# Kernel optimization log

Measured on AMD Instinct MI355X. Metric: run time of the kernel, lower is better.

## Reference

```python
import jax, jax.numpy as jnp
import numpy as np

D_MODEL = 1024
D_FF = 2048
NA = 4
NB = 4
E = NA * NB
B = 2
S = 1024


def setup_inputs() -> dict:
    key = jax.random.key(0)
    ks = jax.random.split(key, 8)
    s = 0.02
    x = jax.random.normal(ks[0], (B, S, D_MODEL), dtype=jnp.float32)
    # stacked per-expert FFN params (torch Linear stored as [in, out] here)
    W1 = (jax.random.normal(ks[1], (E, D_MODEL, 2 * D_FF), dtype=jnp.float32) * s)
    b1 = jnp.zeros((E, 2 * D_FF), dtype=jnp.float32)
    W2 = (jax.random.normal(ks[2], (E, D_FF, D_MODEL), dtype=jnp.float32) * s)
    b2 = jnp.zeros((E, D_MODEL), dtype=jnp.float32)
    Wga = jax.random.normal(ks[3], (D_MODEL, NA), dtype=jnp.float32) * s
    bga = jnp.zeros((NA,), dtype=jnp.float32)
    Wgb = jax.random.normal(ks[4], (D_MODEL, NB), dtype=jnp.float32) * s
    bgb = jnp.zeros((NB,), dtype=jnp.float32)
    return {"x": x, "W1": W1, "b1": b1, "W2": W2, "b2": b2,
            "Wga": Wga, "bga": bga, "Wgb": Wgb, "bgb": bgb}


def reference(x, W1, b1, W2, b2, Wga, bga, Wgb, bgb):
    b, s, d = x.shape
    xf = x.reshape(b * s, d)                     # [T, d]
    probs_A = jax.nn.softmax(xf @ Wga + bga, axis=-1)   # [T, NA]
    probs_B = jax.nn.softmax(xf @ Wgb + bgb, axis=-1)   # [T, NB]
    idx_A = jnp.argmax(probs_A, axis=-1)
    idx_B = jnp.argmax(probs_B, axis=-1)
    oh_A = jax.nn.one_hot(idx_A, NA, dtype=xf.dtype)
    oh_B = jax.nn.one_hot(idx_B, NB, dtype=xf.dtype)
    aux_A = NA * jnp.sum(probs_A.mean(0) * oh_A.mean(0))
    aux_B = NB * jnp.sum(probs_B.mean(0) * oh_B.mean(0))
    total_aux = aux_A + aux_B

    # flattened Cartesian expert index per token
    e_idx = idx_A * NB + idx_B                   # [T]

    # run all experts densely, then select per token (vectorized dispatch)
    h = jnp.einsum('td,edf->etf', xf, W1) + b1[:, None, :]   # [E, T, 2*d_ff]
    a, g = jnp.split(h, 2, axis=-1)
    act = a * jax.nn.silu(g)                                  # [E, T, d_ff]
    y = jnp.einsum('etf,efd->etd', act, W2) + b2[:, None, :]  # [E, T, d]
    oh_E = jax.nn.one_hot(e_idx, E, dtype=xf.dtype)           # [T, E]
    out = jnp.einsum('te,etd->td', oh_E, y)                   # [T, d]
    return out.reshape(b, s, d), total_aux
```

## Files before the change

### kernel.cpp

```cpp
#include <hip/hip_runtime.h>
#include <cstdint>
#include <cstddef>

#define TOKENS 2048
#define DM 1024
#define DFF 2048
#define HC 4096
#define NE 16
#define BM 128

typedef __bf16 bf16x8 __attribute__((ext_vector_type(8)));
typedef float floatx4 __attribute__((ext_vector_type(4)));

static __device__ __forceinline__ unsigned short f2bf(float f) {
    union { float f; unsigned int u; } v; v.f = f;
    unsigned int r = v.u + 0x7fffu + ((v.u >> 16) & 1u);
    return (unsigned short)(r >> 16);
}

union BF8 { bf16x8 v; unsigned short u[8]; };

__global__ __launch_bounds__(256) void moe_gating(
    const float* __restrict__ x, const float* __restrict__ Wga, const float* __restrict__ bga,
    const float* __restrict__ Wgb, const float* __restrict__ bgb,
    float* __restrict__ probsA, float* __restrict__ probsB, int* __restrict__ e_idx)
{
    int wv = threadIdx.x >> 6, lane = threadIdx.x & 63;
    int t = blockIdx.x * 4 + wv;
    const float* xr = x + (size_t)t * DM;
    double aA[4] = {0.,0.,0.,0.}, aB[4] = {0.,0.,0.,0.};
    for (int k = lane; k < DM; k += 64) {
        double xv = (double)xr[k];
        float4 wa = *(const float4*)(Wga + k * 4);
        float4 wb = *(const float4*)(Wgb + k * 4);
        aA[0] += xv * wa.x; aA[1] += xv * wa.y; aA[2] += xv * wa.z; aA[3] += xv * wa.w;
        aB[0] += xv * wb.x; aB[1] += xv * wb.y; aB[2] += xv * wb.z; aB[3] += xv * wb.w;
    }
    #pragma unroll
    for (int off = 32; off >= 1; off >>= 1) {
        #pragma unroll
        for (int j = 0; j < 4; ++j) {
            aA[j] += __shfl_xor(aA[j], off);
            aB[j] += __shfl_xor(aB[j], off);
        }
    }
    if (lane == 0) {
        double lA[4], lB[4];
        #pragma unroll
        for (int j = 0; j < 4; ++j) {
            lA[j] = aA[j] + (double)bga[j];
            lB[j] = aB[j] + (double)bgb[j];
        }
        int ia = 0, ib = 0;
        #pragma unroll
        for (int j = 1; j < 4; ++j) {
            if (lA[j] > lA[ia]) ia = j;
            if (lB[j] > lB[ib]) ib = j;
        }
        double sA = 0., sB = 0., pA[4], pB[4];
        #pragma unroll
        for (int j = 0; j < 4; ++j) {
            pA[j] = exp(lA[j] - lA[ia]); sA += pA[j];
            pB[j] = exp(lB[j] - lB[ib]); sB += pB[j];
        }
        float4 oa, ob;
        oa.x = (float)(pA[0]/sA); oa.y = (float)(pA[1]/sA);
        oa.z = (float)(pA[2]/sA); oa.w = (float)(pA[3]/sA);
        ob.x = (float)(pB[0]/sB); ob.y = (float)(pB[1]/sB);
        ob.z = (float)(pB[2]/sB); ob.w = (float)(pB[3]/sB);
        *(float4*)(probsA + t * 4) = oa;
        *(float4*)(probsB + t * 4) = ob;
        e_idx[t] = ia * 4 + ib;
    }
}

__global__ __launch_bounds__(256) void moe_stats(
    const float* __restrict__ probsA, const float* __restrict__ probsB,
    const int* __restrict__ e_idx,
    int* __restrict__ countE, int* __restrict__ offsets, float* __restrict__ aux_out)
{
    __shared__ float sA[4], sB[4];
    __shared__ int cA[4], cB[4], cE[16];
    int tid = threadIdx.x;
    if (tid < 4) { sA[tid] = 0.f; sB[tid] = 0.f; cA[tid] = 0; cB[tid] = 0; }
    if (tid < 16) cE[tid] = 0;
    __syncthreads();
    float lA[4] = {0,0,0,0}, lB[4] = {0,0,0,0};
    for (int t = tid; t < TOKENS; t += 256) {
        float4 pa = *(const float4*)(probsA + t * 4);
        float4 pb = *(const float4*)(probsB + t * 4);
        lA[0] += pa.x; lA[1] += pa.y; lA[2] += pa.z; lA[3] += pa.w;
        lB[0] += pb.x; lB[1] += pb.y; lB[2] += pb.z; lB[3] += pb.w;
        int e = e_idx[t];
        atomicAdd(&cE[e], 1);
        atomicAdd(&cA[e >> 2], 1);
        atomicAdd(&cB[e & 3], 1);
    }
    #pragma unroll
    for (int j = 0; j < 4; ++j) {
        atomicAdd(&sA[j], lA[j]);
        atomicAdd(&sB[j], lB[j]);
    }
    __syncthreads();
    if (tid == 0) {
        int acc = 0;
        for (int e = 0; e < NE; ++e) { offsets[e] = acc; countE[e] = cE[e]; acc += cE[e]; }
        offsets[NE] = acc;
        float invT = 1.0f / (float)TOKENS;
        float auxA = 0.f, auxB = 0.f;
        for (int j = 0; j < 4; ++j) {
            auxA += (sA[j] * invT) * ((float)cA[j] * invT);
            auxB += (sB[j] * invT) * ((float)cB[j] * invT);
        }
        aux_out[0] = 4.0f * auxA + 4.0f * auxB;
    }
}

__global__ __launch_bounds__(256) void moe_slot(const int* __restrict__ e_idx,
                                                const int* __restrict__ offsets,
                                                int* __restrict__ cursor, int* __restrict__ perm)
{
    int t = blockIdx.x * 256 + threadIdx.x;
    int e = e_idx[t];
    int s = offsets[e] + atomicAdd(&cursor[e], 1);
    perm[s] = t;
}

__global__ __launch_bounds__(256) void moe_gather(const float* __restrict__ x,
                                                  const int* __restrict__ perm,
                                                  unsigned short* __restrict__ Xg)
{
    int s = blockIdx.x;
    int t = perm[s];
    int i = threadIdx.x * 4;
    float4 v = *(const float4*)(x + (size_t)t * DM + i);
    ushort4 o;
    o.x = f2bf(v.x); o.y = f2bf(v.y); o.z = f2bf(v.z); o.w = f2bf(v.w);
    *(ushort4*)(Xg + (size_t)s * DM + i) = o;
}

__global__ __launch_bounds__(256) void moe_ffn1(
    const unsigned short* __restrict__ Xg, const float* __restrict__ W1,
    const float* __restrict__ b1, const int* __restrict__ countE,
    const int* __restrict__ offsets, unsigned short* __restrict__ actbuf)
{
    int e = blockIdx.y;
    int cnt = countE[e];
    if (cnt == 0) return;
    int base = offsets[e];
    int n0 = blockIdx.x * 64;
    __shared__ __align__(16) unsigned short Xs[2 * BM * 40];
    int tid = threadIdx.x, wv = tid >> 6, lane = tid & 63;
    int quad = lane >> 4, l15 = lane & 15;
    const float* W1e = W1 + (size_t)e * DM * HC;
    int col = n0 + wv * 16 + l15;
    const float* pa = W1e + col;
    const float* pg = W1e + DFF + col;
    float ba = b1[e * HC + col];
    float bg = b1[e * HC + DFF + col];
    int row = tid >> 2, kc = tid & 3;

    for (int m0 = blockIdx.z * BM; m0 < cnt; m0 += 2 * BM) {
        floatx4 acc[8][2];
        #pragma unroll
        for (int i = 0; i < 8; ++i) {
            acc[i][0] = floatx4{0.f,0.f,0.f,0.f};
            acc[i][1] = floatx4{0.f,0.f,0.f,0.f};
        }
        #pragma unroll
        for (int p = 0; p < 2; ++p) {
            int r = row + p * 64;
            uint4 v = {0u,0u,0u,0u};
            int m = m0 + r;
            if (m < cnt) v = *(const uint4*)(Xg + (size_t)(base + m) * DM + kc * 8);
            *(uint4*)(Xs + r * 40 + kc * 8) = v;
        }
        float curA[8], curG[8], nxtA[8], nxtG[8];
        {
            const float* qa = pa + (size_t)(quad * 8) * HC;
            const float* qg = pg + (size_t)(quad * 8) * HC;
            #pragma unroll
            for (int j = 0; j < 8; ++j) { curA[j] = qa[(size_t)j * HC]; curG[j] = qg[(size_t)j * HC]; }
        }
        __syncthreads();
        for (int ks = 0; ks < DM / 32; ++ks) {
            int buf = ks & 1;
            if (ks + 1 < DM / 32) {
                int k0n = (ks + 1) * 32;
                #pragma unroll
                for (int p = 0; p < 2; ++p) {
                    int r = row + p * 64;
                    uint4 v = {0u,0u,0u,0u};
                    int m = m0 + r;
                    if (m < cnt) v = *(const uint4*)(Xg + (size_t)(base + m) * DM + k0n + kc * 8);
                    *(uint4*)(Xs + (buf ^ 1) * (BM * 40) + r * 40 + kc * 8) = v;
                }
            }
            bf16x8 af[8];
            #pragma unroll
            for (int i = 0; i < 8; ++i)
                af[i] = *(const bf16x8*)(Xs + buf * (BM * 40) + (i * 16 + l15) * 40 + quad * 8);
            if (ks + 1 < DM / 32) {
                const float* qa = pa + (size_t)((ks + 1) * 32 + quad * 8) * HC;
                const float* qg = pg + (size_t)((ks + 1) * 32 + quad * 8) * HC;
                #pragma unroll
                for (int j = 0; j < 8; ++j) { nxtA[j] = qa[(size_t)j * HC]; nxtG[j] = qg[(size_t)j * HC]; }
            }
            BF8 fa, fg;
            #pragma unroll
            for (int j = 0; j < 8; ++j) { fa.u[j] = f2bf(curA[j]); fg.u[j] = f2bf(curG[j]); }
            #pragma unroll
            for (int i = 0; i < 8; ++i) {
                acc[i][0] = __builtin_amdgcn_mfma_f32_16x16x32_bf16(af[i], fa.v, acc[i][0], 0, 0, 0);
                acc[i][1] = __builtin_amdgcn_mfma_f32_16x16x32_bf16(af[i], fg.v, acc[i][1], 0, 0, 0);
            }
            #pragma unroll
            for (int j = 0; j < 8; ++j) { curA[j] = nxtA[j]; curG[j] = nxtG[j]; }
            __syncthreads();
        }
        #pragma unroll
        for (int i = 0; i < 8; ++i) {
            #pragma unroll
            for (int r = 0; r < 4; ++r) {
                int mr = m0 + i * 16 + quad * 4 + r;
                if (mr < cnt) {
                    float a = acc[i][0][r] + ba;
                    float g = acc[i][1][r] + bg;
                    float sg = 1.0f / (1.0f + __expf(-g));
                    actbuf[(size_t)(base + mr) * DFF + col] = f2bf(a * (g * sg));
                }
            }
        }
    }
}

__global__ __launch_bounds__(256) void moe_ffn2(
    const unsigned short* __restrict__ actbuf, const float* __restrict__ W2,
    const float* __restrict__ b2, const int* __restrict__ countE,
    const int* __restrict__ offsets, const int* __restrict__ perm,
    float* __restrict__ out)
{
    int e = blockIdx.y;
    int cnt = countE[e];
    if (cnt == 0) return;
    int base = offsets[e];
    int n0 = blockIdx.x * 64;
    __shared__ __align__(16) unsigned short As[2 * BM * 40];
    int tid = threadIdx.x, wv = tid >> 6, lane = tid & 63;
    int quad = lane >> 4, l15 = lane & 15;
    const float* W2e = W2 + (size_t)e * DFF * DM;
    int col = n0 + wv * 16 + l15;
    const float* pb = W2e + col;
    float bias = b2[e * DM + col];
    int row = tid >> 2, kc = tid & 3;

    for (int m0 = blockIdx.z * BM; m0 < cnt; m0 += 2 * BM) {
        floatx4 acc[8];
        #pragma unroll
        for (int i = 0; i < 8; ++i) acc[i] = floatx4{0.f,0.f,0.f,0.f};
        #pragma unroll
        for (int p = 0; p < 2; ++p) {
            int r = row + p * 64;
            uint4 v = {0u,0u,0u,0u};
            int m = m0 + r;
            if (m < cnt) v = *(const uint4*)(actbuf + (size_t)(base + m) * DFF + kc * 8);
            *(uint4*)(As + r * 40 + kc * 8) = v;
        }
        float curB[8], nxtB[8];
        {
            const float* qb = pb + (size_t)(quad * 8) * DM;
            #pragma unroll
            for (int j = 0; j < 8; ++j) curB[j] = qb[(size_t)j * DM];
        }
        __syncthreads();
        for (int ks = 0; ks < DFF / 32; ++ks) {
            int buf = ks & 1;
            if (ks + 1 < DFF / 32) {
                int k0n = (ks + 1) * 32;
                #pragma unroll
                for (int p = 0; p < 2; ++p) {
                    int r = row + p * 64;
                    uint4 v = {0u,0u,0u,0u};
                    int m = m0 + r;
                    if (m < cnt) v = *(const uint4*)(actbuf + (size_t)(base + m) * DFF + k0n + kc * 8);
                    *(uint4*)(As + (buf ^ 1) * (BM * 40) + r * 40 + kc * 8) = v;
                }
            }
            bf16x8 af[8];
            #pragma unroll
            for (int i = 0; i < 8; ++i)
                af[i] = *(const bf16x8*)(As + buf * (BM * 40) + (i * 16 + l15) * 40 + quad * 8);
            if (ks + 1 < DFF / 32) {
                const float* qb = pb + (size_t)((ks + 1) * 32 + quad * 8) * DM;
                #pragma unroll
                for (int j = 0; j < 8; ++j) nxtB[j] = qb[(size_t)j * DM];
            }
            BF8 fb;
            #pragma unroll
            for (int j = 0; j < 8; ++j) fb.u[j] = f2bf(curB[j]);
            #pragma unroll
            for (int i = 0; i < 8; ++i)
                acc[i] = __builtin_amdgcn_mfma_f32_16x16x32_bf16(af[i], fb.v, acc[i], 0, 0, 0);
            #pragma unroll
            for (int j = 0; j < 8; ++j) curB[j] = nxtB[j];
            __syncthreads();
        }
        #pragma unroll
        for (int i = 0; i < 8; ++i) {
            #pragma unroll
            for (int r = 0; r < 4; ++r) {
                int mr = m0 + i * 16 + quad * 4 + r;
                if (mr < cnt) {
                    int t = perm[base + mr];
                    out[(size_t)t * DM + col] = acc[i][r] + bias;
                }
            }
        }
    }
}

extern "C" void kernel_launch(void* const* d_in, const int* in_sizes, int n_in,
                              void* d_out, int out_size, void* d_ws, size_t ws_size,
                              hipStream_t stream)
{
    (void)in_sizes; (void)n_in; (void)out_size; (void)ws_size;
    const float* x   = (const float*)d_in[0];
    const float* W1  = (const float*)d_in[1];
    const float* b1  = (const float*)d_in[2];
    const float* W2  = (const float*)d_in[3];
    const float* b2  = (const float*)d_in[4];
    const float* Wga = (const float*)d_in[5];
    const float* bga = (const float*)d_in[6];
    const float* Wgb = (const float*)d_in[7];
    const float* bgb = (const float*)d_in[8];
    float* out = (float*)d_out;

    char* ws = (char*)d_ws;
    int*   countE  = (int*)(ws + 0);
    int*   cursor  = (int*)(ws + 64);
    int*   offsets = (int*)(ws + 256);
    int*   e_idx   = (int*)(ws + 512);
    int*   perm    = (int*)(ws + 8704);
    float* probsA  = (float*)(ws + 16896);
    float* probsB  = (float*)(ws + 49664);
    unsigned short* Xg     = (unsigned short*)(ws + 131072);
    unsigned short* actbuf = (unsigned short*)(ws + (size_t)8 * 1024 * 1024);

    hipMemsetAsync(ws, 0, 256, stream);
    moe_gating<<<TOKENS / 4, 256, 0, stream>>>(x, Wga, bga, Wgb, bgb,
                                               probsA, probsB, e_idx);
    moe_stats<<<1, 256, 0, stream>>>(probsA, probsB, e_idx, countE, offsets,
                                     out + (size_t)TOKENS * DM);
    moe_slot<<<TOKENS / 256, 256, 0, stream>>>(e_idx, offsets, cursor, perm);
    moe_gather<<<TOKENS, 256, 0, stream>>>(x, perm, Xg);
    moe_ffn1<<<dim3(DFF / 64, NE, 2), 256, 0, stream>>>(Xg, W1, b1, countE, offsets, actbuf);
    moe_ffn2<<<dim3(DM / 64, NE, 2), 256, 0, stream>>>(actbuf, W2, b2, countE, offsets, perm, out);
}
```

Baseline: 578.9 us.

## Merge M-split blocks into 512-thread blocks sharing weight loads, defer LDS stores

The grid z-split over token tiles is replaced by a single 512-thread block with a 256-row tile. Two wave groups split the M dimension, so each weight column is fetched once per block instead of once per z-block. The next tile's global loads are now issued before the MFMAs and written to LDS only after them, behind a lighter barrier. bf16 conversion uses native casts instead of the manual rounding helper. The cost is fewer blocks in flight, which lowers parallelism when an expert has few tokens, and more register pressure per block.

```diff
diff --git a/kernel.cpp b/kernel.cpp
--- a/kernel.cpp
+++ b/kernel.cpp
@@ -7,7 +7,7 @@
 #define DFF 2048
 #define HC 4096
 #define NE 16
-#define BM 128
+#define BM 256
 
 typedef __bf16 bf16x8 __attribute__((ext_vector_type(8)));
 typedef float floatx4 __attribute__((ext_vector_type(4)));
@@ -18,7 +18,11 @@
     return (unsigned short)(r >> 16);
 }
 
-union BF8 { bf16x8 v; unsigned short u[8]; };
+static __device__ __forceinline__ void lds_barrier() {
+    asm volatile("s_waitcnt lgkmcnt(0)" ::: "memory");
+    __builtin_amdgcn_s_barrier();
+    __builtin_amdgcn_sched_barrier(0);
+}
 
 __global__ __launch_bounds__(256) void moe_gating(
     const float* __restrict__ x, const float* __restrict__ Wga, const float* __restrict__ bga,
@@ -139,7 +143,7 @@
     *(ushort4*)(Xg + (size_t)s * DM + i) = o;
 }
 
-__global__ __launch_bounds__(256) void moe_ffn1(
+__global__ __launch_bounds__(512) void moe_ffn1(
     const unsigned short* __restrict__ Xg, const float* __restrict__ W1,
     const float* __restrict__ b1, const int* __restrict__ countE,
     const int* __restrict__ offsets, unsigned short* __restrict__ actbuf)
@@ -152,28 +156,29 @@
     __shared__ __align__(16) unsigned short Xs[2 * BM * 40];
     int tid = threadIdx.x, wv = tid >> 6, lane = tid & 63;
     int quad = lane >> 4, l15 = lane & 15;
+    int wvM = wv >> 2, wvN = wv & 3;
     const float* W1e = W1 + (size_t)e * DM * HC;
-    int col = n0 + wv * 16 + l15;
+    int col = n0 + wvN * 16 + l15;
     const float* pa = W1e + col;
     const float* pg = W1e + DFF + col;
     float ba = b1[e * HC + col];
     float bg = b1[e * HC + DFF + col];
     int row = tid >> 2, kc = tid & 3;
 
-    for (int m0 = blockIdx.z * BM; m0 < cnt; m0 += 2 * BM) {
+    for (int m0 = 0; m0 < cnt; m0 += BM) {
         floatx4 acc[8][2];
         #pragma unroll
         for (int i = 0; i < 8; ++i) {
             acc[i][0] = floatx4{0.f,0.f,0.f,0.f};
             acc[i][1] = floatx4{0.f,0.f,0.f,0.f};
         }
-        #pragma unroll
-        for (int p = 0; p < 2; ++p) {
-            int r = row + p * 64;
-            uint4 v = {0u,0u,0u,0u};
-            int m = m0 + r;
-            if (m < cnt) v = *(const uint4*)(Xg + (size_t)(base + m) * DM + kc * 8);
-            *(uint4*)(Xs + r * 40 + kc * 8) = v;
+        {
+            uint4 av0 = {0u,0u,0u,0u}, av1 = {0u,0u,0u,0u};
+            int ma = m0 + row, mb = m0 + row + 128;
+            if (ma < cnt) av0 = *(const uint4*)(Xg + (size_t)(base + ma) * DM + kc * 8);
+            if (mb < cnt) av1 = *(const uint4*)(Xg + (size_t)(base + mb) * DM + kc * 8);
+            *(uint4*)(Xs + row * 40 + kc * 8) = av0;
+            *(uint4*)(Xs + (row + 128) * 40 + kc * 8) = av1;
         }
         float curA[8], curG[8], nxtA[8], nxtG[8];
         {
@@ -182,47 +187,46 @@
             #pragma unroll
             for (int j = 0; j < 8; ++j) { curA[j] = qa[(size_t)j * HC]; curG[j] = qg[(size_t)j * HC]; }
         }
-        __syncthreads();
+        lds_barrier();
         for (int ks = 0; ks < DM / 32; ++ks) {
             int buf = ks & 1;
-            if (ks + 1 < DM / 32) {
+            uint4 nv0 = {0u,0u,0u,0u}, nv1 = {0u,0u,0u,0u};
+            bool more = (ks + 1 < DM / 32);
+            if (more) {
                 int k0n = (ks + 1) * 32;
-                #pragma unroll
-                for (int p = 0; p < 2; ++p) {
-                    int r = row + p * 64;
-                    uint4 v = {0u,0u,0u,0u};
-                    int m = m0 + r;
-                    if (m < cnt) v = *(const uint4*)(Xg + (size_t)(base + m) * DM + k0n + kc * 8);
-                    *(uint4*)(Xs + (buf ^ 1) * (BM * 40) + r * 40 + kc * 8) = v;
-                }
-            }
-            bf16x8 af[8];
-            #pragma unroll
-            for (int i = 0; i < 8; ++i)
-                af[i] = *(const bf16x8*)(Xs + buf * (BM * 40) + (i * 16 + l15) * 40 + quad * 8);
-            if (ks + 1 < DM / 32) {
+                int ma = m0 + row, mb = m0 + row + 128;
+                if (ma < cnt) nv0 = *(const uint4*)(Xg + (size_t)(base + ma) * DM + k0n + kc * 8);
+                if (mb < cnt) nv1 = *(const uint4*)(Xg + (size_t)(base + mb) * DM + k0n + kc * 8);
                 const float* qa = pa + (size_t)((ks + 1) * 32 + quad * 8) * HC;
                 const float* qg = pg + (size_t)((ks + 1) * 32 + quad * 8) * HC;
                 #pragma unroll
                 for (int j = 0; j < 8; ++j) { nxtA[j] = qa[(size_t)j * HC]; nxtG[j] = qg[(size_t)j * HC]; }
             }
-            BF8 fa, fg;
-            #pragma unroll
-            for (int j = 0; j < 8; ++j) { fa.u[j] = f2bf(curA[j]); fg.u[j] = f2bf(curG[j]); }
+            bf16x8 af[8];
+            #pragma unroll
+            for (int i = 0; i < 8; ++i)
+                af[i] = *(const bf16x8*)(Xs + buf * (BM * 40) + (wvM * 128 + i * 16 + l15) * 40 + quad * 8);
+            bf16x8 fa, fg;
+            #pragma unroll
+            for (int j = 0; j < 8; ++j) { fa[j] = (__bf16)curA[j]; fg[j] = (__bf16)curG[j]; }
             #pragma unroll
             for (int i = 0; i < 8; ++i) {
-                acc[i][0] = __builtin_amdgcn_mfma_f32_16x16x32_bf16(af[i], fa.v, acc[i][0], 0, 0, 0);
-                acc[i][1] = __builtin_amdgcn_mfma_f32_16x16x32_bf16(af[i], fg.v, acc[i][1], 0, 0, 0);
-            }
-            #pragma unroll
-            for (int j = 0; j < 8; ++j) { curA[j] = nxtA[j]; curG[j] = nxtG[j]; }
-            __syncthreads();
+                acc[i][0] = __builtin_amdgcn_mfma_f32_16x16x32_bf16(af[i], fa, acc[i][0], 0, 0, 0);
+                acc[i][1] = __builtin_amdgcn_mfma_f32_16x16x32_bf16(af[i], fg, acc[i][1], 0, 0, 0);
+            }
+            if (more) {
+                *(uint4*)(Xs + (buf ^ 1) * (BM * 40) + row * 40 + kc * 8) = nv0;
+                *(uint4*)(Xs + (buf ^ 1) * (BM * 40) + (row + 128) * 40 + kc * 8) = nv1;
+                #pragma unroll
+                for (int j = 0; j < 8; ++j) { curA[j] = nxtA[j]; curG[j] = nxtG[j]; }
+            }
+            lds_barrier();
         }
         #pragma unroll
         for (int i = 0; i < 8; ++i) {
             #pragma unroll
             for (int r = 0; r < 4; ++r) {
-                int mr = m0 + i * 16 + quad * 4 + r;
+                int mr = m0 + wvM * 128 + i * 16 + quad * 4 + r;
                 if (mr < cnt) {
                     float a = acc[i][0][r] + ba;
                     float g = acc[i][1][r] + bg;
@@ -234,7 +238,7 @@
     }
 }
 
-__global__ __launch_bounds__(256) void moe_ffn2(
+__global__ __launch_bounds__(512) void moe_ffn2(
     const unsigned short* __restrict__ actbuf, const float* __restrict__ W2,
     const float* __restrict__ b2, const int* __restrict__ countE,
     const int* __restrict__ offsets, const int* __restrict__ perm,
@@ -248,23 +252,24 @@
     __shared__ __align__(16) unsigned short As[2 * BM * 40];
     int tid = threadIdx.x, wv = tid >> 6, lane = tid & 63;
     int quad = lane >> 4, l15 = lane & 15;
+    int wvM = wv >> 2, wvN = wv & 3;
     const float* W2e = W2 + (size_t)e * DFF * DM;
-    int col = n0 + wv * 16 + l15;
+    int col = n0 + wvN * 16 + l15;
     const float* pb = W2e + col;
     float bias = b2[e * DM + col];
     int row = tid >> 2, kc = tid & 3;
 
-    for (int m0 = blockIdx.z * BM; m0 < cnt; m0 += 2 * BM) {
+    for (int m0 = 0; m0 < cnt; m0 += BM) {
         floatx4 acc[8];
         #pragma unroll
         for (int i = 0; i < 8; ++i) acc[i] = floatx4{0.f,0.f,0.f,0.f};
-        #pragma unroll
-        for (int p = 0; p < 2; ++p) {
-            int r = row + p * 64;
-            uint4 v = {0u,0u,0u,0u};
-            int m = m0 + r;
-            if (m < cnt) v = *(const uint4*)(actbuf + (size_t)(base + m) * DFF + kc * 8);
-            *(uint4*)(As + r * 40 + kc * 8) = v;
+        {
+            uint4 av0 = {0u,0u,0u,0u}, av1 = {0u,0u,0u,0u};
+            int ma = m0 + row, mb = m0 + row + 128;
+            if (ma < cnt) av0 = *(const uint4*)(actbuf + (size_t)(base + ma) * DFF + kc * 8);
+            if (mb < cnt) av1 = *(const uint4*)(actbuf + (size_t)(base + mb) * DFF + kc * 8);
+            *(uint4*)(As + row * 40 + kc * 8) = av0;
+            *(uint4*)(As + (row + 128) * 40 + kc * 8) = av1;
         }
         float curB[8], nxtB[8];
         {
@@ -272,44 +277,43 @@
             #pragma unroll
             for (int j = 0; j < 8; ++j) curB[j] = qb[(size_t)j * DM];
         }
-        __syncthreads();
+        lds_barrier();
         for (int ks = 0; ks < DFF / 32; ++ks) {
             int buf = ks & 1;
-            if (ks + 1 < DFF / 32) {
+            uint4 nv0 = {0u,0u,0u,0u}, nv1 = {0u,0u,0u,0u};
+            bool more = (ks + 1 < DFF / 32);
+            if (more) {
                 int k0n = (ks + 1) * 32;
-                #pragma unroll
-                for (int p = 0; p < 2; ++p) {
-                    int r = row + p * 64;
-                    uint4 v = {0u,0u,0u,0u};
-                    int m = m0 + r;
-                    if (m < cnt) v = *(const uint4*)(actbuf + (size_t)(base + m) * DFF + k0n + kc * 8);
-                    *(uint4*)(As + (buf ^ 1) * (BM * 40) + r * 40 + kc * 8) = v;
-                }
-            }
-            bf16x8 af[8];
-            #pragma unroll
-            for (int i = 0; i < 8; ++i)
-                af[i] = *(const bf16x8*)(As + buf * (BM * 40) + (i * 16 + l15) * 40 + quad * 8);
-            if (ks + 1 < DFF / 32) {
+                int ma = m0 + row, mb = m0 + row + 128;
+                if (ma < cnt) nv0 = *(const uint4*)(actbuf + (size_t)(base + ma) * DFF + k0n + kc * 8);
+                if (mb < cnt) nv1 = *(const uint4*)(actbuf + (size_t)(base + mb) * DFF + k0n + kc * 8);
                 const float* qb = pb + (size_t)((ks + 1) * 32 + quad * 8) * DM;
                 #pragma unroll
                 for (int j = 0; j < 8; ++j) nxtB[j] = qb[(size_t)j * DM];
             }
-            BF8 fb;
-            #pragma unroll
-            for (int j = 0; j < 8; ++j) fb.u[j] = f2bf(curB[j]);
+            bf16x8 af[8];
             #pragma unroll
             for (int i = 0; i < 8; ++i)
-                acc[i] = __builtin_amdgcn_mfma_f32_16x16x32_bf16(af[i], fb.v, acc[i], 0, 0, 0);
-            #pragma unroll
-            for (int j = 0; j < 8; ++j) curB[j] = nxtB[j];
-            __syncthreads();
+                af[i] = *(const bf16x8*)(As + buf * (BM * 40) + (wvM * 128 + i * 16 + l15) * 40 + quad * 8);
+            bf16x8 fb;
+            #pragma unroll
+            for (int j = 0; j < 8; ++j) fb[j] = (__bf16)curB[j];
+            #pragma unroll
+            for (int i = 0; i < 8; ++i)
+                acc[i] = __builtin_amdgcn_mfma_f32_16x16x32_bf16(af[i], fb, acc[i], 0, 0, 0);
+            if (more) {
+                *(uint4*)(As + (buf ^ 1) * (BM * 40) + row * 40 + kc * 8) = nv0;
+                *(uint4*)(As + (buf ^ 1) * (BM * 40) + (row + 128) * 40 + kc * 8) = nv1;
+                #pragma unroll
+                for (int j = 0; j < 8; ++j) curB[j] = nxtB[j];
+            }
+            lds_barrier();
         }
         #pragma unroll
         for (int i = 0; i < 8; ++i) {
             #pragma unroll
             for (int r = 0; r < 4; ++r) {
-                int mr = m0 + i * 16 + quad * 4 + r;
+                int mr = m0 + wvM * 128 + i * 16 + quad * 4 + r;
                 if (mr < cnt) {
                     int t = perm[base + mr];
                     out[(size_t)t * DM + col] = acc[i][r] + bias;
@@ -353,6 +357,6 @@
                                      out + (size_t)TOKENS * DM);
     moe_slot<<<TOKENS / 256, 256, 0, stream>>>(e_idx, offsets, cursor, perm);
     moe_gather<<<TOKENS, 256, 0, stream>>>(x, perm, Xg);
-    moe_ffn1<<<dim3(DFF / 64, NE, 2), 256, 0, stream>>>(Xg, W1, b1, countE, offsets, actbuf);
-    moe_ffn2<<<dim3(DM / 64, NE, 2), 256, 0, stream>>>(actbuf, W2, b2, countE, offsets, perm, out);
-}
+    moe_ffn1<<<dim3(DFF / 64, NE), 512, 0, stream>>>(Xg, W1, b1, countE, offsets, actbuf);
+    moe_ffn2<<<dim3(DM / 64, NE), 512, 0, stream>>>(actbuf, W2, b2, countE, offsets, perm, out);
+}
```

Result: faster. 535.7 us (-7.5%).

## Enlarge FFN GEMM tiles to 256x128 with 512 threads and deeper weight prefetch

Applied to the files above, without the earlier changes.

Both expert FFN kernels now run 512-thread blocks covering 256 token rows and 128 output columns, and the M-split grid dimension is dropped. The block index is remapped so that neighbouring blocks share an expert, which should help L2 reuse of the weights. Weights are prefetched two k-steps ahead, and LDS stores are deferred until after the MFMAs behind a lightweight waitcnt+barrier. The aim is less redundant weight streaming and better latency hiding, at the cost of fewer blocks (256 and 128) and higher register pressure from the doubled accumulators.

```diff
diff --git a/kernel.cpp b/kernel.cpp
--- a/kernel.cpp
+++ b/kernel.cpp
@@ -7,7 +7,7 @@
 #define DFF 2048
 #define HC 4096
 #define NE 16
-#define BM 128
+#define BM 256
 
 typedef __bf16 bf16x8 __attribute__((ext_vector_type(8)));
 typedef float floatx4 __attribute__((ext_vector_type(4)));
@@ -18,7 +18,11 @@
     return (unsigned short)(r >> 16);
 }
 
-union BF8 { bf16x8 v; unsigned short u[8]; };
+static __device__ __forceinline__ void lds_barrier() {
+    asm volatile("s_waitcnt lgkmcnt(0)" ::: "memory");
+    __builtin_amdgcn_s_barrier();
+    __builtin_amdgcn_sched_barrier(0);
+}
 
 __global__ __launch_bounds__(256) void moe_gating(
     const float* __restrict__ x, const float* __restrict__ Wga, const float* __restrict__ bga,
@@ -139,16 +143,19 @@
     *(ushort4*)(Xg + (size_t)s * DM + i) = o;
 }
 
-__global__ __launch_bounds__(256) void moe_ffn1(
+#define NS1 (DM / 32)
+__global__ __launch_bounds__(512, 2) void moe_ffn1(
     const unsigned short* __restrict__ Xg, const float* __restrict__ W1,
     const float* __restrict__ b1, const int* __restrict__ countE,
     const int* __restrict__ offsets, unsigned short* __restrict__ actbuf)
 {
-    int e = blockIdx.y;
+    int id = blockIdx.y * 16 + blockIdx.x;
+    int lid = (id & 7) * 32 + (id >> 3);
+    int e = lid >> 4;
+    int n0 = (lid & 15) * 128;
     int cnt = countE[e];
     if (cnt == 0) return;
     int base = offsets[e];
-    int n0 = blockIdx.x * 64;
     __shared__ __align__(16) unsigned short Xs[2 * BM * 40];
     int tid = threadIdx.x, wv = tid >> 6, lane = tid & 63;
     int quad = lane >> 4, l15 = lane & 15;
@@ -160,66 +167,75 @@
     float bg = b1[e * HC + DFF + col];
     int row = tid >> 2, kc = tid & 3;
 
-    for (int m0 = blockIdx.z * BM; m0 < cnt; m0 += 2 * BM) {
-        floatx4 acc[8][2];
-        #pragma unroll
-        for (int i = 0; i < 8; ++i) {
+    for (int m0 = 0; m0 < cnt; m0 += BM) {
+        floatx4 acc[16][2];
+        #pragma unroll
+        for (int i = 0; i < 16; ++i) {
             acc[i][0] = floatx4{0.f,0.f,0.f,0.f};
             acc[i][1] = floatx4{0.f,0.f,0.f,0.f};
         }
         #pragma unroll
         for (int p = 0; p < 2; ++p) {
-            int r = row + p * 64;
-            uint4 v = {0u,0u,0u,0u};
-            int m = m0 + r;
+            int m = m0 + row + p * 128;
+            uint4 v; v.x = 0u; v.y = 0u; v.z = 0u; v.w = 0u;
             if (m < cnt) v = *(const uint4*)(Xg + (size_t)(base + m) * DM + kc * 8);
-            *(uint4*)(Xs + r * 40 + kc * 8) = v;
-        }
-        float curA[8], curG[8], nxtA[8], nxtG[8];
+            *(uint4*)(Xs + (row + p * 128) * 40 + kc * 8) = v;
+        }
+        float curA[8], curG[8], nxtA[8], nxtG[8], n2A[8], n2G[8];
         {
             const float* qa = pa + (size_t)(quad * 8) * HC;
             const float* qg = pg + (size_t)(quad * 8) * HC;
             #pragma unroll
             for (int j = 0; j < 8; ++j) { curA[j] = qa[(size_t)j * HC]; curG[j] = qg[(size_t)j * HC]; }
-        }
-        __syncthreads();
-        for (int ks = 0; ks < DM / 32; ++ks) {
+            const float* ra = pa + (size_t)(32 + quad * 8) * HC;
+            const float* rg = pg + (size_t)(32 + quad * 8) * HC;
+            #pragma unroll
+            for (int j = 0; j < 8; ++j) { nxtA[j] = ra[(size_t)j * HC]; nxtG[j] = rg[(size_t)j * HC]; }
+        }
+        lds_barrier();
+        for (int ks = 0; ks < NS1; ++ks) {
             int buf = ks & 1;
-            if (ks + 1 < DM / 32) {
+            bool w1 = (ks + 1 < NS1), w2 = (ks + 2 < NS1);
+            uint4 RA[2];
+            if (w1) {
                 int k0n = (ks + 1) * 32;
                 #pragma unroll
                 for (int p = 0; p < 2; ++p) {
-                    int r = row + p * 64;
-                    uint4 v = {0u,0u,0u,0u};
-                    int m = m0 + r;
-                    if (m < cnt) v = *(const uint4*)(Xg + (size_t)(base + m) * DM + k0n + kc * 8);
-                    *(uint4*)(Xs + (buf ^ 1) * (BM * 40) + r * 40 + kc * 8) = v;
+                    int m = m0 + row + p * 128;
+                    RA[p].x = 0u; RA[p].y = 0u; RA[p].z = 0u; RA[p].w = 0u;
+                    if (m < cnt) RA[p] = *(const uint4*)(Xg + (size_t)(base + m) * DM + k0n + kc * 8);
                 }
             }
-            bf16x8 af[8];
-            #pragma unroll
-            for (int i = 0; i < 8; ++i)
-                af[i] = *(const bf16x8*)(Xs + buf * (BM * 40) + (i * 16 + l15) * 40 + quad * 8);
-            if (ks + 1 < DM / 32) {
-                const float* qa = pa + (size_t)((ks + 1) * 32 + quad * 8) * HC;
-                const float* qg = pg + (size_t)((ks + 1) * 32 + quad * 8) * HC;
-                #pragma unroll
-                for (int j = 0; j < 8; ++j) { nxtA[j] = qa[(size_t)j * HC]; nxtG[j] = qg[(size_t)j * HC]; }
-            }
-            BF8 fa, fg;
-            #pragma unroll
-            for (int j = 0; j < 8; ++j) { fa.u[j] = f2bf(curA[j]); fg.u[j] = f2bf(curG[j]); }
-            #pragma unroll
-            for (int i = 0; i < 8; ++i) {
-                acc[i][0] = __builtin_amdgcn_mfma_f32_16x16x32_bf16(af[i], fa.v, acc[i][0], 0, 0, 0);
-                acc[i][1] = __builtin_amdgcn_mfma_f32_16x16x32_bf16(af[i], fg.v, acc[i][1], 0, 0, 0);
-            }
-            #pragma unroll
-            for (int j = 0; j < 8; ++j) { curA[j] = nxtA[j]; curG[j] = nxtG[j]; }
-            __syncthreads();
-        }
-        #pragma unroll
-        for (int i = 0; i < 8; ++i) {
+            if (w2) {
+                const float* qa = pa + (size_t)((ks + 2) * 32 + quad * 8) * HC;
+                const float* qg = pg + (size_t)((ks + 2) * 32 + quad * 8) * HC;
+                #pragma unroll
+                for (int j = 0; j < 8; ++j) { n2A[j] = qa[(size_t)j * HC]; n2G[j] = qg[(size_t)j * HC]; }
+            }
+            bf16x8 fa, fg;
+            #pragma unroll
+            for (int j = 0; j < 8; ++j) { fa[j] = (__bf16)curA[j]; fg[j] = (__bf16)curG[j]; }
+            #pragma unroll
+            for (int i = 0; i < 16; ++i) {
+                bf16x8 af = *(const bf16x8*)(Xs + buf * (BM * 40) + (i * 16 + l15) * 40 + quad * 8);
+                acc[i][0] = __builtin_amdgcn_mfma_f32_16x16x32_bf16(af, fa, acc[i][0], 0, 0, 0);
+                acc[i][1] = __builtin_amdgcn_mfma_f32_16x16x32_bf16(af, fg, acc[i][1], 0, 0, 0);
+            }
+            if (w1) {
+                #pragma unroll
+                for (int p = 0; p < 2; ++p)
+                    *(uint4*)(Xs + (buf ^ 1) * (BM * 40) + (row + p * 128) * 40 + kc * 8) = RA[p];
+                #pragma unroll
+                for (int j = 0; j < 8; ++j) { curA[j] = nxtA[j]; curG[j] = nxtG[j]; }
+            }
+            if (w2) {
+                #pragma unroll
+                for (int j = 0; j < 8; ++j) { nxtA[j] = n2A[j]; nxtG[j] = n2G[j]; }
+            }
+            lds_barrier();
+        }
+        #pragma unroll
+        for (int i = 0; i < 16; ++i) {
             #pragma unroll
             for (int r = 0; r < 4; ++r) {
                 int mr = m0 + i * 16 + quad * 4 + r;
@@ -234,17 +250,20 @@
     }
 }
 
-__global__ __launch_bounds__(256) void moe_ffn2(
+#define NS2 (DFF / 32)
+__global__ __launch_bounds__(512, 2) void moe_ffn2(
     const unsigned short* __restrict__ actbuf, const float* __restrict__ W2,
     const float* __restrict__ b2, const int* __restrict__ countE,
     const int* __restrict__ offsets, const int* __restrict__ perm,
     float* __restrict__ out)
 {
-    int e = blockIdx.y;
+    int id = blockIdx.y * 8 + blockIdx.x;
+    int lid = (id & 7) * 16 + (id >> 3);
+    int e = lid >> 3;
+    int n0 = (lid & 7) * 128;
     int cnt = countE[e];
     if (cnt == 0) return;
     int base = offsets[e];
-    int n0 = blockIdx.x * 64;
     __shared__ __align__(16) unsigned short As[2 * BM * 40];
     int tid = threadIdx.x, wv = tid >> 6, lane = tid & 63;
     int quad = lane >> 4, l15 = lane & 15;
@@ -254,59 +273,68 @@
     float bias = b2[e * DM + col];
     int row = tid >> 2, kc = tid & 3;
 
-    for (int m0 = blockIdx.z * BM; m0 < cnt; m0 += 2 * BM) {
-        floatx4 acc[8];
-        #pragma unroll
-        for (int i = 0; i < 8; ++i) acc[i] = floatx4{0.f,0.f,0.f,0.f};
+    for (int m0 = 0; m0 < cnt; m0 += BM) {
+        floatx4 acc[16];
+        #pragma unroll
+        for (int i = 0; i < 16; ++i) acc[i] = floatx4{0.f,0.f,0.f,0.f};
         #pragma unroll
         for (int p = 0; p < 2; ++p) {
-            int r = row + p * 64;
-            uint4 v = {0u,0u,0u,0u};
-            int m = m0 + r;
+            int m = m0 + row + p * 128;
+            uint4 v; v.x = 0u; v.y = 0u; v.z = 0u; v.w = 0u;
             if (m < cnt) v = *(const uint4*)(actbuf + (size_t)(base + m) * DFF + kc * 8);
-            *(uint4*)(As + r * 40 + kc * 8) = v;
-        }
-        float curB[8], nxtB[8];
+            *(uint4*)(As + (row + p * 128) * 40 + kc * 8) = v;
+        }
+        float curB[8], nxtB[8], n2B[8];
         {
             const float* qb = pb + (size_t)(quad * 8) * DM;
             #pragma unroll
             for (int j = 0; j < 8; ++j) curB[j] = qb[(size_t)j * DM];
-        }
-        __syncthreads();
-        for (int ks = 0; ks < DFF / 32; ++ks) {
+            const float* rb = pb + (size_t)(32 + quad * 8) * DM;
+            #pragma unroll
+            for (int j = 0; j < 8; ++j) nxtB[j] = rb[(size_t)j * DM];
+        }
+        lds_barrier();
+        for (int ks = 0; ks < NS2; ++ks) {
             int buf = ks & 1;
-            if (ks + 1 < DFF / 32) {
+            bool w1 = (ks + 1 < NS2), w2 = (ks + 2 < NS2);
+            uint4 RA[2];
+            if (w1) {
                 int k0n = (ks + 1) * 32;
                 #pragma unroll
                 for (int p = 0; p < 2; ++p) {
-                    int r = row + p * 64;
-                    uint4 v = {0u,0u,0u,0u};
-                    int m = m0 + r;
-                    if (m < cnt) v = *(const uint4*)(actbuf + (size_t)(base + m) * DFF + k0n + kc * 8);
-                    *(uint4*)(As + (buf ^ 1) * (BM * 40) + r * 40 + kc * 8) = v;
+                    int m = m0 + row + p * 128;
+                    RA[p].x = 0u; RA[p].y = 0u; RA[p].z = 0u; RA[p].w = 0u;
+                    if (m < cnt) RA[p] = *(const uint4*)(actbuf + (size_t)(base + m) * DFF + k0n + kc * 8);
                 }
             }
-            bf16x8 af[8];
-            #pragma unroll
-            for (int i = 0; i < 8; ++i)
-                af[i] = *(const bf16x8*)(As + buf * (BM * 40) + (i * 16 + l15) * 40 + quad * 8);
-            if (ks + 1 < DFF / 32) {
-                const float* qb = pb + (size_t)((ks + 1) * 32 + quad * 8) * DM;
-                #pragma unroll
-                for (int j = 0; j < 8; ++j) nxtB[j] = qb[(size_t)j * DM];
-            }
-            BF8 fb;
-            #pragma unroll
-            for (int j = 0; j < 8; ++j) fb.u[j] = f2bf(curB[j]);
-            #pragma unroll
-            for (int i = 0; i < 8; ++i)
-                acc[i] = __builtin_amdgcn_mfma_f32_16x16x32_bf16(af[i], fb.v, acc[i], 0, 0, 0);
-            #pragma unroll
-            for (int j = 0; j < 8; ++j) curB[j] = nxtB[j];
-            __syncthreads();
-        }
-        #pragma unroll
-        for (int i = 0; i < 8; ++i) {
+            if (w2) {
+                const float* qb = pb + (size_t)((ks + 2) * 32 + quad * 8) * DM;
+                #pragma unroll
+                for (int j = 0; j < 8; ++j) n2B[j] = qb[(size_t)j * DM];
+            }
+            bf16x8 fb;
+            #pragma unroll
+            for (int j = 0; j < 8; ++j) fb[j] = (__bf16)curB[j];
+            #pragma unroll
+            for (int i = 0; i < 16; ++i) {
+                bf16x8 af = *(const bf16x8*)(As + buf * (BM * 40) + (i * 16 + l15) * 40 + quad * 8);
+                acc[i] = __builtin_amdgcn_mfma_f32_16x16x32_bf16(af, fb, acc[i], 0, 0, 0);
+            }
+            if (w1) {
+                #pragma unroll
+                for (int p = 0; p < 2; ++p)
+                    *(uint4*)(As + (buf ^ 1) * (BM * 40) + (row + p * 128) * 40 + kc * 8) = RA[p];
+                #pragma unroll
+                for (int j = 0; j < 8; ++j) curB[j] = nxtB[j];
+            }
+            if (w2) {
+                #pragma unroll
+                for (int j = 0; j < 8; ++j) nxtB[j] = n2B[j];
+            }
+            lds_barrier();
+        }
+        #pragma unroll
+        for (int i = 0; i < 16; ++i) {
             #pragma unroll
             for (int r = 0; r < 4; ++r) {
                 int mr = m0 + i * 16 + quad * 4 + r;
@@ -353,6 +381,6 @@
                                      out + (size_t)TOKENS * DM);
     moe_slot<<<TOKENS / 256, 256, 0, stream>>>(e_idx, offsets, cursor, perm);
     moe_gather<<<TOKENS, 256, 0, stream>>>(x, perm, Xg);
-    moe_ffn1<<<dim3(DFF / 64, NE, 2), 256, 0, stream>>>(Xg, W1, b1, countE, offsets, actbuf);
-    moe_ffn2<<<dim3(DM / 64, NE, 2), 256, 0, stream>>>(actbuf, W2, b2, countE, offsets, perm, out);
-}
+    moe_ffn1<<<dim3(16, NE), 512, 0, stream>>>(Xg, W1, b1, countE, offsets, actbuf);
+    moe_ffn2<<<dim3(8, NE), 512, 0, stream>>>(actbuf, W2, b2, countE, offsets, perm, out);
+}
```

Result: faster. 554.6 us (-4.2%).
